# Kernel optimization log

Measured on AMD Instinct MI355X. Metric: run time of the kernel, lower is better.

## Reference

```python
import jax, jax.numpy as jnp
import numpy as np
import math

EMBED_DIM = 1024
NUM_HEADS = 16
NUM_KV_HEADS = 16
DEPTH = 12
HEAD_DIM = EMBED_DIM // NUM_HEADS // 2  # 32
LAMBDA_INIT = 0.8 - 0.6 * math.exp(-0.3 * DEPTH)
EPS = 1e-5
THETA = 0.0001


def rope(q):
    # q: (b, s, h, d) with interleaved pairs, matches apply_rotary_pos_emb
    b, s, h, d = q.shape
    pos = jnp.arange(s, dtype=jnp.float32)[:, None]                      # (s,1)
    freq = 1.0 / (THETA ** (2.0 * jnp.arange(d // 2, dtype=jnp.float32) / d))
    ang = pos * freq                                                     # (s, d/2)
    cos = jnp.cos(ang)[None, :, None, :].astype(q.dtype)
    sin = jnp.sin(ang)[None, :, None, :].astype(q.dtype)
    qr = q.reshape(b, s, h, d // 2, 2)
    q0, q1 = qr[..., 0], qr[..., 1]
    out = jnp.stack([q0 * cos - q1 * sin, q0 * sin + q1 * cos], axis=-1)
    return out.reshape(q.shape)


def setup_inputs() -> dict:
    key = jax.random.key(0)
    ks = jax.random.split(key, 10)
    d = EMBED_DIM
    sd = 1.0 / math.sqrt(d)
    return {
        "x": jax.random.normal(ks[0], (1, 2048, d), dtype=jnp.float32),
        "Wq": jax.random.normal(ks[1], (d, d), dtype=jnp.float32) * sd,
        "Wk": jax.random.normal(ks[2], (d, d), dtype=jnp.float32) * sd,
        "Wv": jax.random.normal(ks[3], (d, d), dtype=jnp.float32) * sd,
        "Wo": jax.random.normal(ks[4], (d, d), dtype=jnp.float32) * sd,
        "lambda_q1": jax.random.normal(ks[5], (HEAD_DIM,), dtype=jnp.float32) * 0.1,
        "lambda_k1": jax.random.normal(ks[6], (HEAD_DIM,), dtype=jnp.float32) * 0.1,
        "lambda_q2": jax.random.normal(ks[7], (HEAD_DIM,), dtype=jnp.float32) * 0.1,
        "lambda_k2": jax.random.normal(ks[8], (HEAD_DIM,), dtype=jnp.float32) * 0.1,
        "subln_g": jnp.ones((2 * HEAD_DIM,), dtype=jnp.float32),
    }


def reference(x, Wq, Wk, Wv, Wo, lambda_q1, lambda_k1, lambda_q2, lambda_k2, subln_g):
    b, s, d = x.shape
    H, hd = NUM_HEADS, HEAD_DIM
    scaling = hd ** (-0.5)

    q = (x @ Wq).reshape(b, s, 2 * H, hd)
    k = (x @ Wk).reshape(b, s, 2 * NUM_KV_HEADS, hd)
    v = (x @ Wv).reshape(b, s, NUM_KV_HEADS, 2 * hd)

    q = rope(q).transpose(0, 2, 1, 3) * scaling   # (b, 2H, s, hd)
    k = rope(k).transpose(0, 2, 1, 3)             # (b, 2H, s, hd)  (n_rep = 1)
    v = v.transpose(0, 2, 1, 3)                   # (b, H, s, 2hd)

    scores = jnp.einsum("bhqd,bhkd->bhqk", q, k)  # (b, 2H, s, s)
    probs = jax.nn.softmax(scores.astype(jnp.float32), axis=-1).astype(scores.dtype)

    lam1 = jnp.exp(jnp.sum(lambda_q1 * lambda_k1))
    lam2 = jnp.exp(jnp.sum(lambda_q2 * lambda_k2))
    lam = (lam1 - lam2 + LAMBDA_INIT).astype(q.dtype)

    probs = probs.reshape(b, H, 2, s, s)
    w = probs[:, :, 0] - lam * probs[:, :, 1]     # (b, H, s, s)

    attn = jnp.einsum("bhqk,bhkd->bhqd", w, v)    # (b, H, s, 2hd)
    rms = jax.lax.rsqrt(jnp.mean(attn * attn, axis=-1, keepdims=True) + EPS)
    attn = attn * rms * subln_g
    attn = attn * (1.0 - LAMBDA_INIT)

    attn = attn.transpose(0, 2, 1, 3).reshape(b, s, H * 2 * hd)
    return attn @ Wo
```

## Files before the change

### kernel.cpp

```cpp
#include <hip/hip_runtime.h>
#include <math.h>

#define S 2048
#define D 1024
#define NH 16
#define HD 32
#define HD2 64

static constexpr float SCALE_Q_EXP2  = 0.17677669529663687f * 1.4426950408889634f;
static constexpr float LAMBDA_INIT_F = 0.78360576653162450f;
static constexpr float ONE_MINUS_LI  = 0.21639423346837553f;

typedef unsigned short u16;
typedef unsigned int   u32;
typedef __attribute__((ext_vector_type(4)))  unsigned short u16x4;
typedef __attribute__((ext_vector_type(8)))  short          bfrag;
typedef __attribute__((ext_vector_type(16))) float          f16acc;
typedef __attribute__((ext_vector_type(4)))  unsigned int   uint4v;

__device__ __forceinline__ u16 f2bf(float f) {
    u32 u = __builtin_bit_cast(u32, f);
    return (u16)((u + 0x7FFFu + ((u >> 16) & 1u)) >> 16);
}
__device__ __forceinline__ f16acc fillv(float v) {
    f16acc z;
#pragma unroll
    for (int i = 0; i < 16; ++i) z[i] = v;
    return z;
}
__device__ __forceinline__ float exp2_raw(float x) {
#if __has_builtin(__builtin_amdgcn_exp2f)
    return __builtin_amdgcn_exp2f(x);
#else
    float r;
    asm volatile("v_exp_f32 %0, %1\n\ts_nop 1" : "=v"(r) : "v"(x));
    return r;
#endif
}
#define MFMA(a, b, c) __builtin_amdgcn_mfma_f32_32x32x16_bf16(a, b, c, 0, 0, 0)

__device__ __forceinline__ void gload16(const u16* src, u16* lds) {
    __builtin_amdgcn_global_load_lds((const __attribute__((address_space(1))) void*)src,
                                     (__attribute__((address_space(3))) void*)lds, 16, 0, 0);
}

__global__ __launch_bounds__(256)
void convert_kernel(const float* __restrict__ x,  const float* __restrict__ Wq,
                    const float* __restrict__ Wk, const float* __restrict__ Wv,
                    const float* __restrict__ Wo,
                    const float* __restrict__ lq1, const float* __restrict__ lk1,
                    const float* __restrict__ lq2, const float* __restrict__ lk2,
                    u16* __restrict__ xb,  u16* __restrict__ WqT, u16* __restrict__ WkT,
                    u16* __restrict__ WvT, u16* __restrict__ WoT,
                    float* __restrict__ cosT, float* __restrict__ sinT,
                    float* __restrict__ lamOut) {
    const int z = blockIdx.y;
    if (z == 0) {
        const int i = blockIdx.x * 256 + threadIdx.x;
        const float4 v = *(const float4*)&x[(size_t)i * 4];
        u16x4 r; r.x = f2bf(v.x); r.y = f2bf(v.y); r.z = f2bf(v.z); r.w = f2bf(v.w);
        *(u16x4*)&xb[(size_t)i * 4] = r;
        return;
    }
    if (z == 5) {
        const int idx = blockIdx.x * 256 + threadIdx.x;
        if (idx < S * 16) {
            int p = idx >> 4;
            int m = idx & 15;
            const double base = (double)1.0e-4f;
            float pf   = (float)pow(base, (double)m * (1.0 / 16.0));
            float freq = 1.0f / pf;
            float angf = (float)p * freq;
            double a = (double)angf;
            cosT[idx] = (float)cos(a);
            sinT[idx] = (float)sin(a);
        }
        if (blockIdx.x == 0 && threadIdx.x == 0) {
            float s1 = 0.f, s2 = 0.f;
            for (int i = 0; i < HD; ++i) {
                s1 += lq1[i] * lk1[i];
                s2 += lq2[i] * lk2[i];
            }
            *lamOut = expf(s1) - expf(s2) + LAMBDA_INIT_F;
        }
        return;
    }
    const int b = blockIdx.x;
    if (b >= 256) return;
    __shared__ u16 Ts[64][66];
    const float* W = (z == 1) ? Wq : (z == 2) ? Wk : (z == 3) ? Wv : Wo;
    u16* T = (z == 1) ? WqT : (z == 2) ? WkT : (z == 3) ? WvT : WoT;
    const int k0 = (b >> 4) * 64, n0 = (b & 15) * 64;
    const int rg = threadIdx.x >> 4, cc = (threadIdx.x & 15) * 4;
#pragma unroll
    for (int i = 0; i < 4; ++i) {
        const int r = rg * 4 + i;
        const float4 v = *(const float4*)&W[(size_t)(k0 + r) * D + n0 + cc];
        Ts[r][cc + 0] = f2bf(v.x); Ts[r][cc + 1] = f2bf(v.y);
        Ts[r][cc + 2] = f2bf(v.z); Ts[r][cc + 3] = f2bf(v.w);
    }
    __syncthreads();
#pragma unroll
    for (int i = 0; i < 4; ++i) {
        const int rn = rg * 4 + i;
        u16x4 res;
        res.x = Ts[cc + 0][rn]; res.y = Ts[cc + 1][rn];
        res.z = Ts[cc + 2][rn]; res.w = Ts[cc + 3][rn];
        *(u16x4*)&T[(size_t)(n0 + rn) * D + k0 + cc] = res;
    }
}

template<int MODE>
__global__ __launch_bounds__(256)
void mm_kernel(const u16* __restrict__ Ab, const u16* __restrict__ B0,
               const u16* __restrict__ B1, const u16* __restrict__ B2,
               const float* __restrict__ cosT, const float* __restrict__ sinT,
               u16* __restrict__ Qb, u16* __restrict__ Kb2, u16* __restrict__ VT,
               float* __restrict__ Of) {
    __shared__ u16 As[64 * 32];
    __shared__ u16 Bs[128 * 32];

    int nb, row0;
    if (MODE == 0) {
        const int lid = blockIdx.x;
        const int xcd = lid & 7;
        const int pos = lid >> 3;
        const int nw  = xcd * 96 + pos;
        nb   = nw >> 5;
        row0 = (nw & 31) * 64;
    } else {
        nb   = blockIdx.x;
        row0 = blockIdx.y * 64;
    }
    const int tid  = threadIdx.x;
    const int wave = tid >> 6;
    const int lane = tid & 63;
    const int ql   = lane & 31;
    const int hi   = lane >> 5;
    const int wr   = wave >> 1;
    const int wc   = wave & 1;

    const u16* Bt;
    int col0B;
    if (MODE == 0) {
        Bt = (nb < 8) ? B0 : (nb < 16) ? B1 : B2;
        col0B = (nb & 7) * 128;
    } else {
        Bt = B0;
        col0B = nb * 128;
    }

    const int rIn = tid >> 2;
    const int kof = 8 * (tid & 3);
    const size_t aRow  = (size_t)(row0 + rIn) * D + kof;
    const size_t bRow0 = (size_t)(col0B + rIn) * D + kof;
    const size_t bRow1 = (size_t)(col0B + 64 + rIn) * D + kof;
    u16* ldsA  = &As[8 * tid];
    u16* ldsB0 = &Bs[8 * tid];
    u16* ldsB1 = &Bs[2048 + 8 * tid];

    const int aoff  = (wr * 32 + ql) * 32 + hi * 8;
    const int boff0 = (wc * 64 + ql) * 32 + hi * 8;
    const int boff1 = (wc * 64 + 32 + ql) * 32 + hi * 8;

    f16acc acc0 = fillv(0.f), acc1 = fillv(0.f);

    for (int kk = 0; kk < D; kk += 32) {
        gload16(Ab + aRow + kk, ldsA);
        gload16(Bt + bRow0 + kk, ldsB0);
        gload16(Bt + bRow1 + kk, ldsB1);
        __syncthreads();
#pragma unroll
        for (int ks = 0; ks < 2; ++ks) {
            const bfrag a  = *(const bfrag*)&As[aoff + ks * 16];
            const bfrag b0 = *(const bfrag*)&Bs[boff0 + ks * 16];
            const bfrag b1 = *(const bfrag*)&Bs[boff1 + ks * 16];
            acc0 = MFMA(a, b0, acc0);
            acc1 = MFMA(a, b1, acc1);
        }
        __syncthreads();
    }

    f16acc accA[2];
    accA[0] = acc0; accA[1] = acc1;

    if (MODE == 0 && nb < 8) {
        const int m = ql >> 1;
        const bool ev = (ql & 1) == 0;
#pragma unroll
        for (int j = 0; j < 2; ++j) {
            const int n = (nb & 7) * 128 + wc * 64 + j * 32 + ql;
            const int head = n >> 5;
            u16* hb = Qb + (size_t)head * S * HD;
#pragma unroll
            for (int r = 0; r < 16; ++r) {
                const int row = row0 + wr * 32 + 4 * hi + (r & 3) + 8 * (r >> 2);
                const float self = accA[j][r];
                const float part = __shfl_xor(self, 1);
                const float c = cosT[(row << 4) + m], s = sinT[(row << 4) + m];
                const float res = ev ? (self * c - part * s) : (part * s + self * c);
                hb[(size_t)row * HD + ql] = f2bf(res * SCALE_Q_EXP2);
            }
        }
    } else if (MODE == 0 && nb < 16) {
        const int m = ql >> 1;
        const bool ev = (ql & 1) == 0;
#pragma unroll
        for (int j = 0; j < 2; ++j) {
            const int n = (nb & 7) * 128 + wc * 64 + j * 32 + ql;
            const int h2 = n >> 5;
            const int d  = n & 31;
            const int dpl = (d >> 3) * 256 + (d & 7);
            u16* hb = Kb2 + (size_t)h2 * 65536;
#pragma unroll
            for (int r = 0; r < 16; ++r) {
                const int row = row0 + wr * 32 + 4 * hi + (r & 3) + 8 * (r >> 2);
                const float self = accA[j][r];
                const float part = __shfl_xor(self, 1);
                const float c = cosT[(row << 4) + m], s = sinT[(row << 4) + m];
                const float res = ev ? (self * c - part * s) : (part * s + self * c);
                hb[(row >> 5) * 1024 + dpl + (row & 31) * 8] = f2bf(res);
            }
        }
    } else if (MODE == 0) {
#pragma unroll
        for (int j = 0; j < 2; ++j) {
            const int n = (nb & 7) * 128 + wc * 64 + j * 32 + ql;
            const int head = n >> 6, d = n & 63;
            const int dt = d >> 5, dl = d & 31;
            u16* tb = VT + (size_t)head * 131072;
#pragma unroll
            for (int q = 0; q < 4; ++q) {
                const int row = row0 + wr * 32 + 4 * hi + 8 * q;
                const int idx = (row >> 5) * 2048 + (dt * 4 + q) * 256 + dl * 8 + 4 * hi;
                u16x4 res;
                res.x = f2bf(accA[j][4 * q + 0]);
                res.y = f2bf(accA[j][4 * q + 1]);
                res.z = f2bf(accA[j][4 * q + 2]);
                res.w = f2bf(accA[j][4 * q + 3]);
                *(u16x4*)&tb[idx] = res;
            }
        }
    } else {
#pragma unroll
        for (int j = 0; j < 2; ++j) {
            const int gcol = col0B + wc * 64 + j * 32 + ql;
#pragma unroll
            for (int r = 0; r < 16; ++r) {
                const int row = row0 + wr * 32 + 4 * hi + (r & 3) + 8 * (r >> 2);
                Of[(size_t)row * D + gcol] = accA[j][r];
            }
        }
    }
}

__global__ __launch_bounds__(512, 2)
void attn_mfma(const u16* __restrict__ Qb, const u16* __restrict__ Kb2,
               const u16* __restrict__ Vt2, const float* __restrict__ lamPtr,
               const float* __restrict__ g, u16* __restrict__ AO) {
    const int bid  = blockIdx.x;
    const int h    = (bid & 7) * 2 + ((bid >> 3) >> 5);
    const int bx   = (bid >> 3) & 31;
    const int tid  = threadIdx.x;
    const int wave = tid >> 6;
    const int lane = tid & 63;
    const int hi   = lane >> 5;
    const int ql   = lane & 31;
    const int t    = wave >> 2;
    const int wv   = wave & 3;
    const int q0   = (bx * 2 + t) * 32;
    const int cbase = wv * 16;

    __shared__ float CMB[2][64][66];

    const u16* qp1 = Qb + ((size_t)(2 * h) * S + q0 + ql) * HD + 8 * hi;
    const u16* qp2 = qp1 + (size_t)S * HD;
    bfrag qf1[2], qf2[2];
    qf1[0] = *(const bfrag*)(qp1);      qf1[1] = *(const bfrag*)(qp1 + 16);
    qf2[0] = *(const bfrag*)(qp2);      qf2[1] = *(const bfrag*)(qp2 + 16);

    const u16* k1g = Kb2 + (size_t)(2 * h) * 65536;
    const u16* k2g = k1g + 65536;
    const u16* vg  = Vt2 + (size_t)h * 131072;
    const int kro  = ql * 8;

    const f16acc ZR = fillv(0.f);
    uint4v ou; ou[0] = ou[1] = ou[2] = ou[3] = 0x3F803F80u;
    const bfrag ONES = __builtin_bit_cast(bfrag, ou);

    f16acc acc1[2], acc2[2];
    acc1[0] = fillv(0.f); acc1[1] = fillv(0.f);
    acc2[0] = fillv(0.f); acc2[1] = fillv(0.f);
    float l1 = 0.f, l2 = 0.f;

    bfrag kA1[2], kA2[2], kB1[2], kB2[2];
    bfrag vA[2][2], vB[2][2];
#pragma unroll
    for (int s = 0; s < 2; ++s) {
        kA1[s] = *(const bfrag*)(k1g + (size_t)cbase * 1024 + (2 * s + hi) * 256 + kro);
        kA2[s] = *(const bfrag*)(k2g + (size_t)cbase * 1024 + (2 * s + hi) * 256 + kro);
#pragma unroll
        for (int dt = 0; dt < 2; ++dt)
            vA[s][dt] = *(const bfrag*)(vg + (size_t)cbase * 2048 + (dt * 4 + 2 * s + hi) * 256 + kro);
    }

    auto body = [&](bfrag (&kc1)[2], bfrag (&kc2)[2], bfrag (&vc)[2][2],
                    bfrag (&kn1)[2], bfrag (&kn2)[2], bfrag (&vn)[2][2], int cn) {
        const u16* k1c = k1g + (size_t)cn * 1024;
        const u16* k2c = k2g + (size_t)cn * 1024;
        const u16* vvc = vg + (size_t)cn * 2048;
#pragma unroll
        for (int s = 0; s < 2; ++s) {
            kn1[s] = *(const bfrag*)(k1c + (2 * s + hi) * 256 + kro);
            kn2[s] = *(const bfrag*)(k2c + (2 * s + hi) * 256 + kro);
#pragma unroll
            for (int dt = 0; dt < 2; ++dt)
                vn[s][dt] = *(const bfrag*)(vvc + (dt * 4 + 2 * s + hi) * 256 + kro);
        }

        __builtin_amdgcn_s_setprio(1);
        f16acc s1 = MFMA(kc1[0], qf1[0], ZR);  s1 = MFMA(kc1[1], qf1[1], s1);
        f16acc s2 = MFMA(kc2[0], qf2[0], ZR);  s2 = MFMA(kc2[1], qf2[1], s2);
        __builtin_amdgcn_s_setprio(0);

#pragma unroll
        for (int r = 0; r < 16; ++r) s1[r] = exp2_raw(s1[r]);
        u32 w1[8];
#pragma unroll
        for (int j = 0; j < 8; ++j)
            asm("v_cvt_pk_bf16_f32 %0, %1, %2" : "=v"(w1[j]) : "v"(s1[2 * j]), "v"(s1[2 * j + 1]));
        asm("v_permlane32_swap_b32 %0, %1" : "+v"(w1[0]), "+v"(w1[2]));
        asm("v_permlane32_swap_b32 %0, %1" : "+v"(w1[1]), "+v"(w1[3]));
        asm("v_permlane32_swap_b32 %0, %1" : "+v"(w1[4]), "+v"(w1[6]));
        asm("v_permlane32_swap_b32 %0, %1" : "+v"(w1[5]), "+v"(w1[7]));
        uint4v u;
        bfrag p1[2];
        u[0] = w1[0]; u[1] = w1[1]; u[2] = w1[2]; u[3] = w1[3];
        p1[0] = __builtin_bit_cast(bfrag, u);
        u[0] = w1[4]; u[1] = w1[5]; u[2] = w1[6]; u[3] = w1[7];
        p1[1] = __builtin_bit_cast(bfrag, u);

        __builtin_amdgcn_s_setprio(1);
        acc1[0] = MFMA(vc[0][0], p1[0], acc1[0]);
        acc1[0] = MFMA(vc[1][0], p1[1], acc1[0]);
        acc1[1] = MFMA(vc[0][1], p1[0], acc1[1]);
        acc1[1] = MFMA(vc[1][1], p1[1], acc1[1]);
        f16acc t1 = MFMA(ONES, p1[0], ZR);  t1 = MFMA(ONES, p1[1], t1);
        __builtin_amdgcn_s_setprio(0);

#pragma unroll
        for (int r = 0; r < 16; ++r) s2[r] = exp2_raw(s2[r]);
        u32 w2[8];
#pragma unroll
        for (int j = 0; j < 8; ++j)
            asm("v_cvt_pk_bf16_f32 %0, %1, %2" : "=v"(w2[j]) : "v"(s2[2 * j]), "v"(s2[2 * j + 1]));
        asm("v_permlane32_swap_b32 %0, %1" : "+v"(w2[0]), "+v"(w2[2]));
        asm("v_permlane32_swap_b32 %0, %1" : "+v"(w2[1]), "+v"(w2[3]));
        asm("v_permlane32_swap_b32 %0, %1" : "+v"(w2[4]), "+v"(w2[6]));
        asm("v_permlane32_swap_b32 %0, %1" : "+v"(w2[5]), "+v"(w2[7]));
        bfrag p2[2];
        u[0] = w2[0]; u[1] = w2[1]; u[2] = w2[2]; u[3] = w2[3];
        p2[0] = __builtin_bit_cast(bfrag, u);
        u[0] = w2[4]; u[1] = w2[5]; u[2] = w2[6]; u[3] = w2[7];
        p2[1] = __builtin_bit_cast(bfrag, u);

        __builtin_amdgcn_s_setprio(1);
        acc2[0] = MFMA(vc[0][0], p2[0], acc2[0]);
        acc2[0] = MFMA(vc[1][0], p2[1], acc2[0]);
        acc2[1] = MFMA(vc[0][1], p2[0], acc2[1]);
        acc2[1] = MFMA(vc[1][1], p2[1], acc2[1]);
        f16acc t2 = MFMA(ONES, p2[0], ZR);  t2 = MFMA(ONES, p2[1], t2);
        __builtin_amdgcn_s_setprio(0);

        l1 += t1[0];
        l2 += t2[0];
    };

    for (int i = 0; i < 16; i += 2) {
        const int c0 = cbase + i;
        body(kA1, kA2, vA, kB1, kB2, vB, c0 + 1);
        const int c2 = (i + 2 < 16) ? c0 + 2 : c0 + 1;
        body(kB1, kB2, vB, kA1, kA2, vA, c2);
    }

#pragma unroll 1
    for (int p = 1; p < 4; ++p) {
        if (wv == p) {
            float* c0 = &CMB[t][lane][0];
#pragma unroll
            for (int dt = 0; dt < 2; ++dt)
#pragma unroll
                for (int r = 0; r < 16; ++r) {
                    c0[dt * 16 + r]      = acc1[dt][r];
                    c0[32 + dt * 16 + r] = acc2[dt][r];
                }
            c0[64] = l1; c0[65] = l2;
        }
        __syncthreads();
        if (wv == 0) {
            const float* c0 = &CMB[t][lane][0];
#pragma unroll
            for (int dt = 0; dt < 2; ++dt)
#pragma unroll
                for (int r = 0; r < 16; ++r) {
                    acc1[dt][r] += c0[dt * 16 + r];
                    acc2[dt][r] += c0[32 + dt * 16 + r];
                }
            l1 += c0[64]; l2 += c0[65];
        }
        __syncthreads();
    }

    if (wv == 0) {
        const float lam = *lamPtr;
        const float inv1 = 1.0f / l1, inv2 = 1.0f / l2;
        float o_[2][16];
        float ss = 0.f;
#pragma unroll
        for (int dt = 0; dt < 2; ++dt)
#pragma unroll
            for (int r = 0; r < 16; ++r) {
                float o = acc1[dt][r] * inv1 - lam * (acc2[dt][r] * inv2);
                o_[dt][r] = o;
                ss += o * o;
            }
        ss += __shfl_xor(ss, 32);
        const float rs = rsqrtf(ss * (1.0f / 64.0f) + 1e-5f);

        u16* aorow = AO + (size_t)(q0 + ql) * D + h * 64;
#pragma unroll
        for (int dt = 0; dt < 2; ++dt)
#pragma unroll
            for (int G = 0; G < 4; ++G) {
                const int dbase = dt * 32 + G * 8 + hi * 4;
                const float4 gv = *(const float4*)&g[dbase];
                u16x4 res;
                res.x = f2bf(o_[dt][4 * G + 0] * rs * gv.x * ONE_MINUS_LI);
                res.y = f2bf(o_[dt][4 * G + 1] * rs * gv.y * ONE_MINUS_LI);
                res.z = f2bf(o_[dt][4 * G + 2] * rs * gv.z * ONE_MINUS_LI);
                res.w = f2bf(o_[dt][4 * G + 3] * rs * gv.w * ONE_MINUS_LI);
                *(u16x4*)&aorow[dbase] = res;
            }
    }
}

extern "C" void kernel_launch(void* const* d_in, const int* in_sizes, int n_in,
                              void* d_out, int out_size, void* d_ws, size_t ws_size,
                              hipStream_t stream) {
    const float* x   = (const float*)d_in[0];
    const float* Wq  = (const float*)d_in[1];
    const float* Wk  = (const float*)d_in[2];
    const float* Wv  = (const float*)d_in[3];
    const float* Wo  = (const float*)d_in[4];
    const float* lq1 = (const float*)d_in[5];
    const float* lk1 = (const float*)d_in[6];
    const float* lq2 = (const float*)d_in[7];
    const float* lk2 = (const float*)d_in[8];
    const float* g   = (const float*)d_in[9];
    float* out = (float*)d_out;

    char* ws = (char*)d_ws;
    float* cosT = (float*)(ws);
    float* sinT = (float*)(ws + 131072);
    float* lam  = (float*)(ws + 262144);
    char*  b    = ws + 262400;
    u16*   Qb   = (u16*)(b);
    u16*   Kb2  = (u16*)(b + 4194304);
    u16*   VT   = (u16*)(b + 8388608);
    u16*   AO   = (u16*)(b + 12582912);
    u16*   xb   = (u16*)(b + 16777216);
    u16*   WqT  = (u16*)(b + 20971520);
    u16*   WkT  = (u16*)(b + 23068672);
    u16*   WvT  = (u16*)(b + 25165824);
    u16*   WoT  = (u16*)(b + 27262976);

    convert_kernel<<<dim3(2048, 6), 256, 0, stream>>>(x, Wq, Wk, Wv, Wo,
                                                      lq1, lk1, lq2, lk2,
                                                      xb, WqT, WkT, WvT, WoT,
                                                      cosT, sinT, lam);

    mm_kernel<0><<<768, 256, 0, stream>>>(xb, WqT, WkT, WvT, cosT, sinT,
                                          Qb, Kb2, VT, nullptr);

    attn_mfma<<<512, 512, 0, stream>>>(Qb, Kb2, VT, lam, g, AO);

    mm_kernel<1><<<dim3(8, 32), 256, 0, stream>>>(AO, WoT, nullptr, nullptr, cosT, sinT,
                                                  nullptr, nullptr, nullptr, out);
}
```

Before: 96.57 us.

## Software-pipeline QK^T MFMAs one chunk ahead of softmax and PV

Restructures the attention inner loop so the score MFMAs for the next key chunk are issued right after the current chunk's PV MFMAs. Each s1/s2 is computed ahead of time and overlaps with the exp2/convert work of the other branch. K fragments are now single-buffered because they are consumed right after loading, which lowers register pressure. The risk is that the next chunk's score MFMAs now wait on the global loads issued in the same iteration, so some load latency may be exposed.

```diff
diff --git a/kernel.cpp b/kernel.cpp
--- a/kernel.cpp
+++ b/kernel.cpp
@@ -293,35 +293,35 @@
     acc2[0] = fillv(0.f); acc2[1] = fillv(0.f);
     float l1 = 0.f, l2 = 0.f;
 
-    bfrag kA1[2], kA2[2], kB1[2], kB2[2];
+    bfrag kn1[2], kn2[2];
     bfrag vA[2][2], vB[2][2];
+    f16acc s1, s2;
+
 #pragma unroll
     for (int s = 0; s < 2; ++s) {
-        kA1[s] = *(const bfrag*)(k1g + (size_t)cbase * 1024 + (2 * s + hi) * 256 + kro);
-        kA2[s] = *(const bfrag*)(k2g + (size_t)cbase * 1024 + (2 * s + hi) * 256 + kro);
+        kn1[s] = *(const bfrag*)(k1g + (size_t)cbase * 1024 + (2 * s + hi) * 256 + kro);
+        kn2[s] = *(const bfrag*)(k2g + (size_t)cbase * 1024 + (2 * s + hi) * 256 + kro);
 #pragma unroll
         for (int dt = 0; dt < 2; ++dt)
             vA[s][dt] = *(const bfrag*)(vg + (size_t)cbase * 2048 + (dt * 4 + 2 * s + hi) * 256 + kro);
     }
-
-    auto body = [&](bfrag (&kc1)[2], bfrag (&kc2)[2], bfrag (&vc)[2][2],
-                    bfrag (&kn1)[2], bfrag (&kn2)[2], bfrag (&vn)[2][2], int cn) {
-        const u16* k1c = k1g + (size_t)cn * 1024;
-        const u16* k2c = k2g + (size_t)cn * 1024;
-        const u16* vvc = vg + (size_t)cn * 2048;
-#pragma unroll
-        for (int s = 0; s < 2; ++s) {
-            kn1[s] = *(const bfrag*)(k1c + (2 * s + hi) * 256 + kro);
-            kn2[s] = *(const bfrag*)(k2c + (2 * s + hi) * 256 + kro);
-#pragma unroll
-            for (int dt = 0; dt < 2; ++dt)
-                vn[s][dt] = *(const bfrag*)(vvc + (dt * 4 + 2 * s + hi) * 256 + kro);
-        }
-
-        __builtin_amdgcn_s_setprio(1);
-        f16acc s1 = MFMA(kc1[0], qf1[0], ZR);  s1 = MFMA(kc1[1], qf1[1], s1);
-        f16acc s2 = MFMA(kc2[0], qf2[0], ZR);  s2 = MFMA(kc2[1], qf2[1], s2);
-        __builtin_amdgcn_s_setprio(0);
+    s1 = MFMA(kn1[0], qf1[0], ZR);  s1 = MFMA(kn1[1], qf1[1], s1);
+    s2 = MFMA(kn2[0], qf2[0], ZR);  s2 = MFMA(kn2[1], qf2[1], s2);
+
+    auto body = [&](bfrag (&vc)[2][2], bfrag (&vn)[2][2], int cn, bool more) {
+        if (more) {
+            const u16* k1c = k1g + (size_t)cn * 1024;
+            const u16* k2c = k2g + (size_t)cn * 1024;
+            const u16* vvc = vg + (size_t)cn * 2048;
+#pragma unroll
+            for (int s = 0; s < 2; ++s) {
+                kn1[s] = *(const bfrag*)(k1c + (2 * s + hi) * 256 + kro);
+                kn2[s] = *(const bfrag*)(k2c + (2 * s + hi) * 256 + kro);
+#pragma unroll
+                for (int dt = 0; dt < 2; ++dt)
+                    vn[s][dt] = *(const bfrag*)(vvc + (dt * 4 + 2 * s + hi) * 256 + kro);
+            }
+        }
 
 #pragma unroll
         for (int r = 0; r < 16; ++r) s1[r] = exp2_raw(s1[r]);
@@ -348,6 +348,10 @@
         f16acc t1 = MFMA(ONES, p1[0], ZR);  t1 = MFMA(ONES, p1[1], t1);
         __builtin_amdgcn_s_setprio(0);
 
+        if (more) {
+            s1 = MFMA(kn1[0], qf1[0], ZR);  s1 = MFMA(kn1[1], qf1[1], s1);
+        }
+
 #pragma unroll
         for (int r = 0; r < 16; ++r) s2[r] = exp2_raw(s2[r]);
         u32 w2[8];
@@ -372,15 +376,18 @@
         f16acc t2 = MFMA(ONES, p2[0], ZR);  t2 = MFMA(ONES, p2[1], t2);
         __builtin_amdgcn_s_setprio(0);
 
+        if (more) {
+            s2 = MFMA(kn2[0], qf2[0], ZR);  s2 = MFMA(kn2[1], qf2[1], s2);
+        }
+
         l1 += t1[0];
         l2 += t2[0];
     };
 
     for (int i = 0; i < 16; i += 2) {
-        const int c0 = cbase + i;
-        body(kA1, kA2, vA, kB1, kB2, vB, c0 + 1);
-        const int c2 = (i + 2 < 16) ? c0 + 2 : c0 + 1;
-        body(kB1, kB2, vB, kA1, kA2, vA, c2);
+        body(vA, vB, cbase + i + 1, true);
+        const bool more = (i + 2 < 16);
+        body(vB, vA, more ? cbase + i + 2 : 0, more);
     }
 
 #pragma unroll 1
```

After: 97.83 us. No clear change (+1.3%).
